# Kernel tuning notes

Measured on AMD Instinct MI355X. Metric: run time of the kernel, lower is better.

Reference implementation:

```python
import jax, jax.numpy as jnp
import numpy as np

T, B, N, D, H = 128, 64, 24, 256, 8
F = D // H  # 32


def setup_inputs() -> dict:
    key = jax.random.key(0)
    ks = jax.random.split(key, 7)
    s = 1.0 / np.sqrt(D)  # torch nn.Linear default init range
    inputs = jax.random.normal(ks[0], (T, B, N * D), dtype=jnp.float32)
    Wk = jax.random.uniform(ks[1], (H, F, D), minval=-s, maxval=s, dtype=jnp.float32)
    bk = jax.random.uniform(ks[2], (H, F), minval=-s, maxval=s, dtype=jnp.float32)
    Wv = jax.random.uniform(ks[3], (H, F, D), minval=-s, maxval=s, dtype=jnp.float32)
    bv = jax.random.uniform(ks[4], (H, F), minval=-s, maxval=s, dtype=jnp.float32)
    Wq = jax.random.uniform(ks[5], (H, N, F, D), minval=-s, maxval=s, dtype=jnp.float32)
    bq = jax.random.uniform(ks[6], (H, N, F), minval=-s, maxval=s, dtype=jnp.float32)
    return {"inputs": inputs, "Wk": Wk, "bk": bk, "Wv": Wv, "bv": bv, "Wq": Wq, "bq": bq}


def reference(inputs, Wk, bk, Wv, bv, Wq, bq):
    # inputs: (T, B, N*D) -> (T, B, N, D)
    x = inputs.reshape(T, B, N, D)
    # shared K/V per head: (T, B, H, N, F)
    k = jnp.einsum('tbnd,hfd->tbhnf', x, Wk) + bk[:, None, :]
    v = jnp.einsum('tbnd,hfd->tbhnf', x, Wv) + bv[:, None, :]
    # per-joint Q: joint n uses its own (F, D) weight -> (T, B, H, N, F)
    q = jnp.einsum('tbnd,hnfd->tbhnf', x, Wq) + bq
    # attention over joints, scaled by sqrt(F)
    scores = jnp.einsum('tbhnf,tbhmf->tbhnm', q, k) / jnp.sqrt(jnp.float32(F))
    attn = jax.nn.softmax(scores, axis=-1)
    out = jnp.einsum('tbhnm,tbhmf->tbhnf', attn, v)
    # concat heads along feature dim per joint, then flatten joints: (T, B, N*H*F)
    out = out.transpose(0, 1, 3, 2, 4).reshape(T, B, N * H * F)
    # dropout is identity in eval mode
    return out
```

## Files before the change

### kernel.cpp

```cpp
#include <hip/hip_runtime.h>
#include <hip/hip_bf16.h>
#include <cstdio>

#define TB  8192
#define N_  24
#define D_  256
#define H_  8
#define F_  32
#define ND  6144
#define HNF 6144

typedef unsigned short u16;
typedef __attribute__((ext_vector_type(8))) _Float16 f16x8;
typedef __attribute__((ext_vector_type(8))) short bf16x8;
typedef __attribute__((ext_vector_type(4))) float f32x4;

__device__ __forceinline__ u16 f2b(float f) {
    unsigned int u = __float_as_uint(f);
    return (u16)((u + 0x7FFFu + ((u >> 16) & 1u)) >> 16);
}
__device__ __forceinline__ float b2f(u16 s) {
    return __uint_as_float(((unsigned int)s) << 16);
}
__device__ __forceinline__ u16 f2h(float f) {
    _Float16 h = (_Float16)f;
    u16 u; __builtin_memcpy(&u, &h, 2); return u;
}

__device__ __forceinline__ void gl_lds16(const void* g, void* l) {
    __builtin_amdgcn_global_load_lds(
        (const __attribute__((address_space(1))) unsigned int*)g,
        (__attribute__((address_space(3))) unsigned int*)l, 16, 0, 0);
}

__global__ __launch_bounds__(256) void prep_weights(
    const float* __restrict__ Wk, const float* __restrict__ Wv,
    const float* __restrict__ Wq, u16* __restrict__ Bp)
{
    const int idx = blockIdx.x * 256 + threadIdx.x;
    if (idx >= 24 * 8 * 48 * 64) return;
    const int fr = idx & 15;
    const int fq = (idx >> 4) & 3;
    const int g  = (idx >> 6) % 48;
    const int kt = (idx / (64 * 48)) % 8;
    const int n  = idx / (64 * 48 * 8);
    const int col = g * 16 + fr;
    const int d0  = kt * 32 + fq * 8;
    const int c   = col & 255;
    const float* src;
    if (col < 256)      src = Wk + (size_t)c * 256 + d0;
    else if (col < 512) src = Wv + (size_t)c * 256 + d0;
    else {
        const int h = c >> 5, f = c & 31;
        src = Wq + ((size_t)(h * 24 + n) * 32 + f) * 256 + d0;
    }
    __align__(16) u16 out[8];
    #pragma unroll
    for (int j = 0; j < 8; ++j) out[j] = f2h(src[j]);
    *reinterpret_cast<uint4*>(Bp + (size_t)idx * 8) =
        *reinterpret_cast<const uint4*>(out);
}

__global__ __launch_bounds__(256) void prep_bias(
    const float* __restrict__ bk, const float* __restrict__ bv,
    const float* __restrict__ bq, float* __restrict__ biasp)
{
    const int idx = blockIdx.x * 256 + threadIdx.x;
    if (idx >= 24 * 768) return;
    const int col = idx % 768, n = idx / 768;
    const int c = col & 255;
    float v;
    if (col < 256)      v = bk[c];
    else if (col < 512) v = bv[c];
    else { const int h = c >> 5, f = c & 31; v = bq[(h * 24 + n) * 32 + f]; }
    biasp[n * 768 + col] = v;
}

__global__ __launch_bounds__(512, 4) void proj_mfma(
    const float* __restrict__ x,
    const u16* __restrict__ Bp,
    const float* __restrict__ biasp,
    u16* __restrict__ kb, u16* __restrict__ vb, u16* __restrict__ qb)
{
    const int b    = blockIdx.x;
    const int xcd  = b & 7;
    const int t    = b >> 3;
    const int gi   = t % 9;
    const int mblk = t / 9;
    const int grp  = xcd * 9 + gi;
    const int n    = grp / 3;
    const int ct   = grp % 3;
    const int tb0  = mblk * 128;
    const int tid  = threadIdx.x;
    const int w    = tid >> 6;
    const int lane = tid & 63;
    const int wm   = w >> 2;
    const int wn   = w & 3;
    const int fr   = lane & 15, fq = lane >> 4;

    __shared__ __align__(16) char smem[49152];
    char* const Ab = smem;
    char* const Bb = smem + 16384;

    const int arow = tid >> 2;
    const int ac   = tid & 3;
    const float* xsrc = x + (size_t)(tb0 + arow) * ND + n * 256 + ac * 8;
    const int awbyte = arow * 64 + ((ac ^ ((arow >> 1) & 3)) << 4);

    const size_t bbase = (size_t)(n * 8 * 48 + ct * 16 + w * 2) * 1024 + lane * 16;

    f32x4 acc[4][4];
    #pragma unroll
    for (int m = 0; m < 4; ++m)
        #pragma unroll
        for (int j = 0; j < 4; ++j) acc[m][j] = (f32x4){0.f, 0.f, 0.f, 0.f};

    float4 axr[2][2];

    axr[0][0] = *reinterpret_cast<const float4*>(xsrc);
    axr[0][1] = *reinterpret_cast<const float4*>(xsrc + 4);
    gl_lds16((const char*)Bp + bbase,        Bb + (w * 2) * 1024);
    gl_lds16((const char*)Bp + bbase + 1024, Bb + (w * 2 + 1) * 1024);
    asm volatile("s_waitcnt vmcnt(2)" ::: "memory");
    {
        ushort4 hv, hv2;
        hv.x  = f2h(axr[0][0].x); hv.y  = f2h(axr[0][0].y);
        hv.z  = f2h(axr[0][0].z); hv.w  = f2h(axr[0][0].w);
        hv2.x = f2h(axr[0][1].x); hv2.y = f2h(axr[0][1].y);
        hv2.z = f2h(axr[0][1].z); hv2.w = f2h(axr[0][1].w);
        *reinterpret_cast<ushort4*>(Ab + awbyte)     = hv;
        *reinterpret_cast<ushort4*>(Ab + awbyte + 8) = hv2;
    }
    axr[1][0] = *reinterpret_cast<const float4*>(xsrc + 32);
    axr[1][1] = *reinterpret_cast<const float4*>(xsrc + 36);
    asm volatile("s_waitcnt lgkmcnt(0)" ::: "memory");
    asm volatile("s_waitcnt vmcnt(2)" ::: "memory");
    __builtin_amdgcn_s_barrier();
    asm volatile("" ::: "memory");

    #pragma unroll
    for (int kt = 0; kt < 8; ++kt) {
        const int c = kt & 1, o = c ^ 1;

        if (kt < 7) {
            const size_t bs = bbase + (size_t)(kt + 1) * 48 * 1024;
            gl_lds16((const char*)Bp + bs,        Bb + o * 16384 + (w * 2) * 1024);
            gl_lds16((const char*)Bp + bs + 1024, Bb + o * 16384 + (w * 2 + 1) * 1024);
        }

        f16x8 bfr[4], afr[4];
        #pragma unroll
        for (int j = 0; j < 4; ++j)
            bfr[j] = *reinterpret_cast<const f16x8*>(
                Bb + c * 16384 + (wn * 4 + j) * 1024 + lane * 16);
        #pragma unroll
        for (int m = 0; m < 4; ++m) {
            const int row = wm * 64 + m * 16 + fr;
            afr[m] = *reinterpret_cast<const f16x8*>(
                Ab + c * 8192 + row * 64 + ((fq ^ ((fr >> 1) & 3)) << 4));
        }
        __builtin_amdgcn_s_setprio(1);
        #pragma unroll
        for (int j = 0; j < 4; ++j)
            #pragma unroll
            for (int m = 0; m < 4; ++m)
                acc[m][j] = __builtin_amdgcn_mfma_f32_16x16x32_f16(
                    afr[m], bfr[j], acc[m][j], 0, 0, 0);
        __builtin_amdgcn_s_setprio(0);

        if (kt < 7) {
            asm volatile("s_waitcnt vmcnt(2)" ::: "memory");
            __builtin_amdgcn_sched_barrier(0);
            {
                const float4 lo = axr[(kt + 1) & 1][0];
                const float4 hi = axr[(kt + 1) & 1][1];
                ushort4 hv, hv2;
                hv.x  = f2h(lo.x); hv.y  = f2h(lo.y); hv.z  = f2h(lo.z); hv.w  = f2h(lo.w);
                hv2.x = f2h(hi.x); hv2.y = f2h(hi.y); hv2.z = f2h(hi.z); hv2.w = f2h(hi.w);
                *reinterpret_cast<ushort4*>(Ab + o * 8192 + awbyte)     = hv;
                *reinterpret_cast<ushort4*>(Ab + o * 8192 + awbyte + 8) = hv2;
            }
            if (kt < 6) {
                axr[kt & 1][0] = *reinterpret_cast<const float4*>(xsrc + (kt + 2) * 32);
                axr[kt & 1][1] = *reinterpret_cast<const float4*>(xsrc + (kt + 2) * 32 + 4);
            }
            asm volatile("s_waitcnt lgkmcnt(0)" ::: "memory");
            if (kt < 6) {
                asm volatile("s_waitcnt vmcnt(2)" ::: "memory");
            } else {
                asm volatile("s_waitcnt vmcnt(0)" ::: "memory");
            }
            __builtin_amdgcn_s_barrier();
            asm volatile("" ::: "memory");
        }
    }
    __syncthreads();

    u16* dst = (ct == 0) ? kb : (ct == 1) ? vb : qb;
    #pragma unroll
    for (int p = 0; p < 2; ++p) {
        if (wm == p) {
            #pragma unroll
            for (int j = 0; j < 4; ++j) {
                const int colL = wn * 64 + j * 16 + fr;
                const float bs = biasp[n * 768 + ct * 256 + colL];
                #pragma unroll
                for (int m = 0; m < 4; ++m)
                    #pragma unroll
                    for (int r = 0; r < 4; ++r) {
                        const int rowL = m * 16 + fq * 4 + r;
                        const int byte = (rowL * 512 + colL * 2) ^ ((rowL & 7) << 4);
                        *reinterpret_cast<u16*>(smem + byte) = f2b(acc[m][j][r] + bs);
                    }
            }
        }
        __syncthreads();
        #pragma unroll
        for (int it = 0; it < 4; ++it) {
            const int id  = it * 512 + tid;
            const int row = id >> 5;
            const int cch = id & 31;
            const uint4 v = *reinterpret_cast<const uint4*>(
                smem + ((row * 512 + cch * 16) ^ ((row & 7) << 4)));
            *reinterpret_cast<uint4*>(
                &dst[(size_t)(tb0 + p * 64 + row) * HNF + n * 256 + cch * 8]) = v;
        }
        __syncthreads();
    }
}

__device__ __forceinline__ int swz(int row, int chunk) {
    return row * 32 + (((chunk ^ ((row >> 1) ^ (row >> 3))) & 3) << 3);
}

__global__ __launch_bounds__(256) void attn_mfma(
    const u16* __restrict__ kb,
    const u16* __restrict__ vb,
    const u16* __restrict__ qb,
    float* __restrict__ out)
{
    const int tid  = threadIdx.x;
    const int wid  = tid >> 6;
    const int lane = tid & 63;
    const int fr   = lane & 15;
    const int fq   = lane >> 4;
    const size_t tb = (size_t)blockIdx.x * 4 + wid;

    __shared__ __align__(16) u16 lds[4][2048];
    u16* Pw = lds[wid];
    u16* Vt = lds[wid] + 1024;

    #pragma unroll
    for (int i = 0; i < 4; ++i)
        reinterpret_cast<uint4*>(lds[wid])[lane + i * 64] = (uint4){0, 0, 0, 0};

    const u16* qt = qb + tb * HNF;
    const u16* kt = kb + tb * HNF;
    const u16* vt = vb + tb * HNF;
    float* outp = out + tb * ND;

    const float scale = 0.17677669529663687f;
    const bool colok = fr < 8;

    for (int h = 0; h < H_; ++h) {
        const u16* qh = qt + h * 32;
        const u16* kh = kt + h * 32;
        const u16* vh = vt + h * 32;

        bf16x8 qa[2], ka[2];
        #pragma unroll
        for (int t = 0; t < 2; ++t) {
            int rq = t * 16 + fr; rq = rq < 24 ? rq : 23;
            qa[t] = *reinterpret_cast<const bf16x8*>(qh + rq * 256 + fq * 8);
            ka[t] = *reinterpret_cast<const bf16x8*>(kh + rq * 256 + fq * 8);
        }

        {
            const int m = lane >> 2, q = lane & 3;
            const uint4 vv = *reinterpret_cast<const uint4*>(vh + m * 256 + q * 8);
            #pragma unroll
            for (int j = 0; j < 8; ++j) {
                const int f = q * 8 + j;
                Vt[swz(f, m >> 3) + (m & 7)] = reinterpret_cast<const u16*>(&vv)[j];
            }
            if (lane < 32) {
                const int m2 = 16 + (lane >> 2), q2 = lane & 3;
                const uint4 v2 = *reinterpret_cast<const uint4*>(vh + m2 * 256 + q2 * 8);
                #pragma unroll
                for (int j = 0; j < 8; ++j) {
                    const int f = q2 * 8 + j;
                    Vt[swz(f, m2 >> 3) + (m2 & 7)] = reinterpret_cast<const u16*>(&v2)[j];
                }
            }
        }

        f32x4 S[2][2];
        #pragma unroll
        for (int a = 0; a < 2; ++a)
            #pragma unroll
            for (int bb = 0; bb < 2; ++bb)
                S[a][bb] = __builtin_amdgcn_mfma_f32_16x16x32_bf16(
                    qa[a], ka[bb], (f32x4){0.f, 0.f, 0.f, 0.f}, 0, 0, 0);

        float inv[2][4];
        #pragma unroll
        for (int t = 0; t < 2; ++t) {
            float e0[4], e1[4];
            #pragma unroll
            for (int r = 0; r < 4; ++r) {
                const float a = S[t][0][r] * scale;
                const float bbv = colok ? S[t][1][r] * scale : -1e30f;
                float mx = fmaxf(a, bbv);
                #pragma unroll
                for (int off = 1; off < 16; off <<= 1)
                    mx = fmaxf(mx, __shfl_xor(mx, off));
                e0[r] = __expf(a - mx);
                e1[r] = colok ? __expf(bbv - mx) : 0.f;
                float sm = e0[r] + e1[r];
                #pragma unroll
                for (int off = 1; off < 16; off <<= 1)
                    sm += __shfl_xor(sm, off);
                inv[t][r] = 1.f / sm;
            }
            #pragma unroll
            for (int r = 0; r < 4; ++r) {
                const int row = t * 16 + fq * 4 + r;
                if (row < 24) {
                    Pw[swz(row, fr >> 3) + (fr & 7)] = f2b(e0[r]);
                    if (colok) {
                        const int c1 = 16 + fr;
                        Pw[swz(row, c1 >> 3) + (c1 & 7)] = f2b(e1[r]);
                    }
                }
            }
        }

        bf16x8 pa[2], vbf[2];
        #pragma unroll
        for (int t = 0; t < 2; ++t)
            pa[t] = *reinterpret_cast<const bf16x8*>(&Pw[swz(t * 16 + fr, fq)]);
        #pragma unroll
        for (int t = 0; t < 2; ++t)
            vbf[t] = *reinterpret_cast<const bf16x8*>(&Vt[swz(t * 16 + fr, fq)]);

        f32x4 O[2][2];
        #pragma unroll
        for (int a = 0; a < 2; ++a)
            #pragma unroll
            for (int bb = 0; bb < 2; ++bb)
                O[a][bb] = __builtin_amdgcn_mfma_f32_16x16x32_bf16(
                    pa[a], vbf[bb], (f32x4){0.f, 0.f, 0.f, 0.f}, 0, 0, 0);

        #pragma unroll
        for (int a = 0; a < 2; ++a)
            #pragma unroll
            for (int r = 0; r < 4; ++r) {
                const int row = a * 16 + fq * 4 + r;
                if (row < 24) {
                    outp[row * D_ + h * F_ + fr]      = O[a][0][r] * inv[a][r];
                    outp[row * D_ + h * F_ + 16 + fr] = O[a][1][r] * inv[a][r];
                }
            }
    }
}

extern "C" void kernel_launch(void* const* d_in, const int* in_sizes, int n_in,
                              void* d_out, int out_size, void* d_ws, size_t ws_size,
                              hipStream_t stream) {
    const float* x  = (const float*)d_in[0];
    const float* Wk = (const float*)d_in[1];
    const float* bk = (const float*)d_in[2];
    const float* Wv = (const float*)d_in[3];
    const float* bv = (const float*)d_in[4];
    const float* Wq = (const float*)d_in[5];
    const float* bq = (const float*)d_in[6];
    float* out = (float*)d_out;

    const size_t qkv_elems = (size_t)TB * HNF;
    const size_t need = qkv_elems * 2ull * 3ull;
    if (ws_size < need) fprintf(stderr, "ws too small: %zu < %zu\n", ws_size, need);
    u16* kbuf = (u16*)d_ws;
    u16* vbuf = kbuf + qkv_elems;
    u16* qbuf = vbuf + qkv_elems;

    u16*   Bp    = (u16*)d_out;
    float* biasp = (float*)((char*)d_out + (size_t)24 * 8 * 48 * 512 * 2);

    prep_weights<<<2304, 256, 0, stream>>>(Wk, Wv, Wq, Bp);
    prep_bias<<<(24 * 768 + 255) / 256, 256, 0, stream>>>(bk, bv, bq, biasp);
    proj_mfma<<<4608, 512, 0, stream>>>(x, Bp, biasp, kbuf, vbuf, qbuf);
    attn_mfma<<<TB / 4, 256, 0, stream>>>(kbuf, vbuf, qbuf, out);
}
```

Measured before the change: 284.8 us.

## Deepen projection GEMM pipeline to triple-buffered B tiles and three-stage x prefetch

```diff
diff --git a/kernel.cpp b/kernel.cpp
--- a/kernel.cpp
+++ b/kernel.cpp
@@ -98,9 +98,9 @@
     const int wn   = w & 3;
     const int fr   = lane & 15, fq = lane >> 4;
 
-    __shared__ __align__(16) char smem[49152];
+    __shared__ __align__(16) char smem[65536];
     char* const Ab = smem;
-    char* const Bb = smem + 16384;
+    char* const Bbuf = smem + 16384;
 
     const int arow = tid >> 2;
     const int ac   = tid & 3;
@@ -115,13 +115,19 @@
         #pragma unroll
         for (int j = 0; j < 4; ++j) acc[m][j] = (f32x4){0.f, 0.f, 0.f, 0.f};
 
-    float4 axr[2][2];
+    float4 axr[3][2];
 
     axr[0][0] = *reinterpret_cast<const float4*>(xsrc);
     axr[0][1] = *reinterpret_cast<const float4*>(xsrc + 4);
-    gl_lds16((const char*)Bp + bbase,        Bb + (w * 2) * 1024);
-    gl_lds16((const char*)Bp + bbase + 1024, Bb + (w * 2 + 1) * 1024);
-    asm volatile("s_waitcnt vmcnt(2)" ::: "memory");
+    gl_lds16((const char*)Bp + bbase,                Bbuf + (w * 2) * 1024);
+    gl_lds16((const char*)Bp + bbase + 1024,         Bbuf + (w * 2 + 1) * 1024);
+    gl_lds16((const char*)Bp + bbase + 49152,        Bbuf + 16384 + (w * 2) * 1024);
+    gl_lds16((const char*)Bp + bbase + 49152 + 1024, Bbuf + 16384 + (w * 2 + 1) * 1024);
+    axr[1][0] = *reinterpret_cast<const float4*>(xsrc + 32);
+    axr[1][1] = *reinterpret_cast<const float4*>(xsrc + 36);
+    axr[2][0] = *reinterpret_cast<const float4*>(xsrc + 64);
+    axr[2][1] = *reinterpret_cast<const float4*>(xsrc + 68);
+    asm volatile("s_waitcnt vmcnt(8)" ::: "memory");
     {
         ushort4 hv, hv2;
         hv.x  = f2h(axr[0][0].x); hv.y  = f2h(axr[0][0].y);
@@ -131,33 +137,33 @@
         *reinterpret_cast<ushort4*>(Ab + awbyte)     = hv;
         *reinterpret_cast<ushort4*>(Ab + awbyte + 8) = hv2;
     }
-    axr[1][0] = *reinterpret_cast<const float4*>(xsrc + 32);
-    axr[1][1] = *reinterpret_cast<const float4*>(xsrc + 36);
     asm volatile("s_waitcnt lgkmcnt(0)" ::: "memory");
-    asm volatile("s_waitcnt vmcnt(2)" ::: "memory");
+    asm volatile("s_waitcnt vmcnt(6)" ::: "memory");
     __builtin_amdgcn_s_barrier();
     asm volatile("" ::: "memory");
 
     #pragma unroll
     for (int kt = 0; kt < 8; ++kt) {
-        const int c = kt & 1, o = c ^ 1;
-
-        if (kt < 7) {
-            const size_t bs = bbase + (size_t)(kt + 1) * 48 * 1024;
-            gl_lds16((const char*)Bp + bs,        Bb + o * 16384 + (w * 2) * 1024);
-            gl_lds16((const char*)Bp + bs + 1024, Bb + o * 16384 + (w * 2 + 1) * 1024);
+        const int ca = kt & 1, oa = ca ^ 1;
+        const int bk = kt % 3;
+
+        if (kt < 6) {
+            const size_t bs = bbase + (size_t)(kt + 2) * 49152;
+            char* bdst = Bbuf + ((kt + 2) % 3) * 16384;
+            gl_lds16((const char*)Bp + bs,        bdst + (w * 2) * 1024);
+            gl_lds16((const char*)Bp + bs + 1024, bdst + (w * 2 + 1) * 1024);
         }
 
         f16x8 bfr[4], afr[4];
         #pragma unroll
         for (int j = 0; j < 4; ++j)
             bfr[j] = *reinterpret_cast<const f16x8*>(
-                Bb + c * 16384 + (wn * 4 + j) * 1024 + lane * 16);
+                Bbuf + bk * 16384 + (wn * 4 + j) * 1024 + lane * 16);
         #pragma unroll
         for (int m = 0; m < 4; ++m) {
             const int row = wm * 64 + m * 16 + fr;
             afr[m] = *reinterpret_cast<const f16x8*>(
-                Ab + c * 8192 + row * 64 + ((fq ^ ((fr >> 1) & 3)) << 4));
+                Ab + ca * 8192 + row * 64 + ((fq ^ ((fr >> 1) & 3)) << 4));
         }
         __builtin_amdgcn_s_setprio(1);
         #pragma unroll
@@ -169,27 +175,27 @@
         __builtin_amdgcn_s_setprio(0);
 
         if (kt < 7) {
-            asm volatile("s_waitcnt vmcnt(2)" ::: "memory");
+            if (kt == 0)      { asm volatile("s_waitcnt vmcnt(4)" ::: "memory"); }
+            else if (kt == 6) { asm volatile("s_waitcnt vmcnt(2)" ::: "memory"); }
+            else              { asm volatile("s_waitcnt vmcnt(6)" ::: "memory"); }
             __builtin_amdgcn_sched_barrier(0);
             {
-                const float4 lo = axr[(kt + 1) & 1][0];
-                const float4 hi = axr[(kt + 1) & 1][1];
+                const float4 lo = axr[(kt + 1) % 3][0];
+                const float4 hi = axr[(kt + 1) % 3][1];
                 ushort4 hv, hv2;
                 hv.x  = f2h(lo.x); hv.y  = f2h(lo.y); hv.z  = f2h(lo.z); hv.w  = f2h(lo.w);
                 hv2.x = f2h(hi.x); hv2.y = f2h(hi.y); hv2.z = f2h(hi.z); hv2.w = f2h(hi.w);
-                *reinterpret_cast<ushort4*>(Ab + o * 8192 + awbyte)     = hv;
-                *reinterpret_cast<ushort4*>(Ab + o * 8192 + awbyte + 8) = hv2;
-            }
-            if (kt < 6) {
-                axr[kt & 1][0] = *reinterpret_cast<const float4*>(xsrc + (kt + 2) * 32);
-                axr[kt & 1][1] = *reinterpret_cast<const float4*>(xsrc + (kt + 2) * 32 + 4);
+                *reinterpret_cast<ushort4*>(Ab + oa * 8192 + awbyte)     = hv;
+                *reinterpret_cast<ushort4*>(Ab + oa * 8192 + awbyte + 8) = hv2;
+            }
+            if (kt < 5) {
+                axr[kt % 3][0] = *reinterpret_cast<const float4*>(xsrc + (kt + 3) * 32);
+                axr[kt % 3][1] = *reinterpret_cast<const float4*>(xsrc + (kt + 3) * 32 + 4);
             }
             asm volatile("s_waitcnt lgkmcnt(0)" ::: "memory");
-            if (kt < 6) {
-                asm volatile("s_waitcnt vmcnt(2)" ::: "memory");
-            } else {
-                asm volatile("s_waitcnt vmcnt(0)" ::: "memory");
-            }
+            if (kt < 5)       { asm volatile("s_waitcnt vmcnt(6)" ::: "memory"); }
+            else if (kt == 5) { asm volatile("s_waitcnt vmcnt(4)" ::: "memory"); }
+            else              { asm volatile("s_waitcnt vmcnt(0)" ::: "memory"); }
             __builtin_amdgcn_s_barrier();
             asm volatile("" ::: "memory");
         }
```

Measured after the change: 296.6 us. 1.04x slower.

## Store QKV intermediates joint-major and merge weight/bias prep kernels

Applied to the files above, without the earlier changes.

```diff
diff --git a/kernel.cpp b/kernel.cpp
--- a/kernel.cpp
+++ b/kernel.cpp
@@ -33,47 +33,45 @@
         (__attribute__((address_space(3))) unsigned int*)l, 16, 0, 0);
 }
 
-__global__ __launch_bounds__(256) void prep_weights(
+__global__ __launch_bounds__(256) void prep_all(
     const float* __restrict__ Wk, const float* __restrict__ Wv,
-    const float* __restrict__ Wq, u16* __restrict__ Bp)
+    const float* __restrict__ Wq,
+    const float* __restrict__ bk, const float* __restrict__ bv,
+    const float* __restrict__ bq,
+    u16* __restrict__ Bp, float* __restrict__ biasp)
 {
     const int idx = blockIdx.x * 256 + threadIdx.x;
-    if (idx >= 24 * 8 * 48 * 64) return;
-    const int fr = idx & 15;
-    const int fq = (idx >> 4) & 3;
-    const int g  = (idx >> 6) % 48;
-    const int kt = (idx / (64 * 48)) % 8;
-    const int n  = idx / (64 * 48 * 8);
-    const int col = g * 16 + fr;
-    const int d0  = kt * 32 + fq * 8;
-    const int c   = col & 255;
-    const float* src;
-    if (col < 256)      src = Wk + (size_t)c * 256 + d0;
-    else if (col < 512) src = Wv + (size_t)c * 256 + d0;
-    else {
-        const int h = c >> 5, f = c & 31;
-        src = Wq + ((size_t)(h * 24 + n) * 32 + f) * 256 + d0;
-    }
-    __align__(16) u16 out[8];
-    #pragma unroll
-    for (int j = 0; j < 8; ++j) out[j] = f2h(src[j]);
-    *reinterpret_cast<uint4*>(Bp + (size_t)idx * 8) =
-        *reinterpret_cast<const uint4*>(out);
-}
-
-__global__ __launch_bounds__(256) void prep_bias(
-    const float* __restrict__ bk, const float* __restrict__ bv,
-    const float* __restrict__ bq, float* __restrict__ biasp)
-{
-    const int idx = blockIdx.x * 256 + threadIdx.x;
-    if (idx >= 24 * 768) return;
-    const int col = idx % 768, n = idx / 768;
-    const int c = col & 255;
-    float v;
-    if (col < 256)      v = bk[c];
-    else if (col < 512) v = bv[c];
-    else { const int h = c >> 5, f = c & 31; v = bq[(h * 24 + n) * 32 + f]; }
-    biasp[n * 768 + col] = v;
+    if (idx < 24 * 8 * 48 * 64) {
+        const int fr = idx & 15;
+        const int fq = (idx >> 4) & 3;
+        const int g  = (idx >> 6) % 48;
+        const int kt = (idx / (64 * 48)) % 8;
+        const int n  = idx / (64 * 48 * 8);
+        const int col = g * 16 + fr;
+        const int d0  = kt * 32 + fq * 8;
+        const int c   = col & 255;
+        const float* src;
+        if (col < 256)      src = Wk + (size_t)c * 256 + d0;
+        else if (col < 512) src = Wv + (size_t)c * 256 + d0;
+        else {
+            const int h = c >> 5, f = c & 31;
+            src = Wq + ((size_t)(h * 24 + n) * 32 + f) * 256 + d0;
+        }
+        __align__(16) u16 out[8];
+        #pragma unroll
+        for (int j = 0; j < 8; ++j) out[j] = f2h(src[j]);
+        *reinterpret_cast<uint4*>(Bp + (size_t)idx * 8) =
+            *reinterpret_cast<const uint4*>(out);
+    } else if (idx < 24 * 8 * 48 * 64 + 24 * 768) {
+        const int bi  = idx - 24 * 8 * 48 * 64;
+        const int col = bi % 768, n = bi / 768;
+        const int c = col & 255;
+        float v;
+        if (col < 256)      v = bk[c];
+        else if (col < 512) v = bv[c];
+        else { const int h = c >> 5, f = c & 31; v = bq[(h * 24 + n) * 32 + f]; }
+        biasp[n * 768 + col] = v;
+    }
 }
 
 __global__ __launch_bounds__(512, 4) void proj_mfma(
@@ -143,7 +141,7 @@
         const int c = kt & 1, o = c ^ 1;
 
         if (kt < 7) {
-            const size_t bs = bbase + (size_t)(kt + 1) * 48 * 1024;
+            const size_t bs = bbase + (size_t)(kt + 1) * 49152;
             gl_lds16((const char*)Bp + bs,        Bb + o * 16384 + (w * 2) * 1024);
             gl_lds16((const char*)Bp + bs + 1024, Bb + o * 16384 + (w * 2 + 1) * 1024);
         }
@@ -223,7 +221,7 @@
             const uint4 v = *reinterpret_cast<const uint4*>(
                 smem + ((row * 512 + cch * 16) ^ ((row & 7) << 4)));
             *reinterpret_cast<uint4*>(
-                &dst[(size_t)(tb0 + p * 64 + row) * HNF + n * 256 + cch * 8]) = v;
+                &dst[((size_t)n * TB + tb0 + p * 64 + row) * 256 + cch * 8]) = v;
         }
         __syncthreads();
     }
@@ -232,6 +230,8 @@
 __device__ __forceinline__ int swz(int row, int chunk) {
     return row * 32 + (((chunk ^ ((row >> 1) ^ (row >> 3))) & 3) << 3);
 }
+
+#define JS ((size_t)TB * 256)
 
 __global__ __launch_bounds__(256) void attn_mfma(
     const u16* __restrict__ kb,
@@ -254,30 +254,28 @@
     for (int i = 0; i < 4; ++i)
         reinterpret_cast<uint4*>(lds[wid])[lane + i * 64] = (uint4){0, 0, 0, 0};
 
-    const u16* qt = qb + tb * HNF;
-    const u16* kt = kb + tb * HNF;
-    const u16* vt = vb + tb * HNF;
+    const size_t tbo = tb * 256;
     float* outp = out + tb * ND;
 
     const float scale = 0.17677669529663687f;
     const bool colok = fr < 8;
 
     for (int h = 0; h < H_; ++h) {
-        const u16* qh = qt + h * 32;
-        const u16* kh = kt + h * 32;
-        const u16* vh = vt + h * 32;
+        const u16* qh = qb + tbo + h * 32;
+        const u16* kh = kb + tbo + h * 32;
+        const u16* vh = vb + tbo + h * 32;
 
         bf16x8 qa[2], ka[2];
         #pragma unroll
         for (int t = 0; t < 2; ++t) {
             int rq = t * 16 + fr; rq = rq < 24 ? rq : 23;
-            qa[t] = *reinterpret_cast<const bf16x8*>(qh + rq * 256 + fq * 8);
-            ka[t] = *reinterpret_cast<const bf16x8*>(kh + rq * 256 + fq * 8);
+            qa[t] = *reinterpret_cast<const bf16x8*>(qh + (size_t)rq * JS + fq * 8);
+            ka[t] = *reinterpret_cast<const bf16x8*>(kh + (size_t)rq * JS + fq * 8);
         }
 
         {
             const int m = lane >> 2, q = lane & 3;
-            const uint4 vv = *reinterpret_cast<const uint4*>(vh + m * 256 + q * 8);
+            const uint4 vv = *reinterpret_cast<const uint4*>(vh + (size_t)m * JS + q * 8);
             #pragma unroll
             for (int j = 0; j < 8; ++j) {
                 const int f = q * 8 + j;
@@ -285,7 +283,7 @@
             }
             if (lane < 32) {
                 const int m2 = 16 + (lane >> 2), q2 = lane & 3;
-                const uint4 v2 = *reinterpret_cast<const uint4*>(vh + m2 * 256 + q2 * 8);
+                const uint4 v2 = *reinterpret_cast<const uint4*>(vh + (size_t)m2 * JS + q2 * 8);
                 #pragma unroll
                 for (int j = 0; j < 8; ++j) {
                     const int f = q2 * 8 + j;
@@ -386,8 +384,7 @@
     u16*   Bp    = (u16*)d_out;
     float* biasp = (float*)((char*)d_out + (size_t)24 * 8 * 48 * 512 * 2);
 
-    prep_weights<<<2304, 256, 0, stream>>>(Wk, Wv, Wq, Bp);
-    prep_bias<<<(24 * 768 + 255) / 256, 256, 0, stream>>>(bk, bv, bq, biasp);
+    prep_all<<<2376, 256, 0, stream>>>(Wk, Wv, Wq, bk, bv, bq, Bp, biasp);
     proj_mfma<<<4608, 512, 0, stream>>>(x, Bp, biasp, kbuf, vbuf, qbuf);
     attn_mfma<<<TB / 4, 256, 0, stream>>>(kbuf, vbuf, qbuf, out);
 }
```

New measurement: 322.5 us. +13.2%, slower.
